# Performance work log

Measured on AMD Instinct MI355X. Metric: run time of the kernel, lower is better.

## Reference

```python
import jax, jax.numpy as jnp
import numpy as np

D = 4096  # in_features == out_features (required: LayerNorm(in_features) applied to out-dim output)
B, S = 4, 4096
LN_EPS = 1e-5


def setup_inputs() -> dict:
    key = jax.random.key(0)
    ks = jax.random.split(key, 5)
    return {
        "x": jax.random.normal(ks[0], (B, S, D), dtype=jnp.float32),
        "weight": jax.random.normal(ks[1], (D, D), dtype=jnp.float32),  # [out, in]
        "bias": jax.random.normal(ks[2], (D,), dtype=jnp.float32),
        "g": jax.random.normal(ks[3], (D,), dtype=jnp.float32),   # input scale [in]
        "h": jax.random.normal(ks[4], (D,), dtype=jnp.float32),   # output scale [out]
        "ln_gamma": jnp.ones((D,), dtype=jnp.float32),
        "ln_beta": jnp.zeros((D,), dtype=jnp.float32),
    }


def reference(x, weight, bias, g, h, ln_gamma, ln_beta):
    sign_w = jnp.sign(weight)                      # binarized weight [out, in]
    xg = x * g                                     # per-input-channel scale
    y = jnp.einsum("bsi,oi->bso", xg, sign_w) + bias
    y = y * h                                      # per-output-channel scale
    mu = jnp.mean(y, axis=-1, keepdims=True)
    var = jnp.mean(jnp.square(y - mu), axis=-1, keepdims=True)
    out = (y - mu) * jax.lax.rsqrt(var + LN_EPS) * ln_gamma + ln_beta
    return out
```

## Files before the change

### kernel.cpp

```cpp
#include <hip/hip_runtime.h>
#include <hip/hip_bf16.h>
#include <stdint.h>

typedef __bf16 bf16x8 __attribute__((ext_vector_type(8)));
typedef float f32x4 __attribute__((ext_vector_type(4)));

#define GLDS16(gp, lp) __builtin_amdgcn_global_load_lds( \
    (const __attribute__((address_space(1))) unsigned int*)(gp), \
    (__attribute__((address_space(3))) unsigned int*)(lp), 16, 0, 0)

#define BARRIER() asm volatile("s_barrier" ::: "memory")
#define VMCNT(n)  asm volatile("s_waitcnt vmcnt(" #n ")" ::: "memory")


__global__ __launch_bounds__(256) void prep_xg(
    const float* __restrict__ x, const float* __restrict__ g,
    __bf16* __restrict__ out, long total, int K)
{
    long i = ((long)blockIdx.x * blockDim.x + threadIdx.x) * 8;
    const long stride = (long)gridDim.x * blockDim.x * 8;
    for (; i < total; i += stride) {
        const int k = (int)(i & (long)(K - 1));
        f32x4 x0 = *(const f32x4*)(x + i);
        f32x4 x1 = *(const f32x4*)(x + i + 4);
        f32x4 g0 = *(const f32x4*)(g + k);
        f32x4 g1 = *(const f32x4*)(g + k + 4);
        bf16x8 o;
        #pragma unroll
        for (int j = 0; j < 4; ++j) o[j]     = (__bf16)(x0[j] * g0[j]);
        #pragma unroll
        for (int j = 0; j < 4; ++j) o[4 + j] = (__bf16)(x1[j] * g1[j]);
        *(bf16x8*)(out + i) = o;
    }
}

__global__ __launch_bounds__(256) void prep_sign(
    const float* __restrict__ w, __bf16* __restrict__ out, long total)
{
    long i = ((long)blockIdx.x * blockDim.x + threadIdx.x) * 8;
    const long stride = (long)gridDim.x * blockDim.x * 8;
    for (; i < total; i += stride) {
        f32x4 w0 = *(const f32x4*)(w + i);
        f32x4 w1 = *(const f32x4*)(w + i + 4);
        bf16x8 o;
        #pragma unroll
        for (int j = 0; j < 4; ++j)
            o[j]     = (__bf16)((w0[j] > 0.f) ? 1.f : ((w0[j] < 0.f) ? -1.f : 0.f));
        #pragma unroll
        for (int j = 0; j < 4; ++j)
            o[4 + j] = (__bf16)((w1[j] > 0.f) ? 1.f : ((w1[j] < 0.f) ? -1.f : 0.f));
        *(bf16x8*)(out + i) = o;
    }
}


template<bool BF16OUT>
__global__ __launch_bounds__(512, 2) void gemm_r4(
    const __bf16* __restrict__ A, const __bf16* __restrict__ B,
    const float* __restrict__ bias, const float* __restrict__ h,
    __bf16* __restrict__ yb, float* __restrict__ yf, int M, int N, int K)
{
    extern __shared__ __bf16 sm[];

    const int xcd = blockIdx.x & 7;
    const int l = blockIdx.x >> 3;
    const int bn = xcd * 2 + (l & 1);
    const int bm = l >> 1;

    const int t = threadIdx.x;
    const int lane = t & 63;
    const int w = t >> 6;
    const int wm = w >> 2;
    const int wn = w & 3;
    const int sl = lane >> 4;
    const int fr = lane & 15;
    const int swz = (sl ^ ((fr >> 1) & 3)) * 8;

    const int row8 = t >> 2;
    const int chS = ((t & 3) ^ ((t >> 3) & 3)) * 8;

    const __bf16* gA = A + (long)(bm * 256 + row8) * K + chS;
    const __bf16* gB = B + (long)(bn * 256 + row8) * K + chS;

    const int NT = K / 32;

#define STG_A(b, T) do { \
    GLDS16(gA + (long)(T) * 32,            &sm[(b) * 16384 + t * 8]); \
    GLDS16(gA + 128L * K + (long)(T) * 32, &sm[(b) * 16384 + 4096 + t * 8]); \
} while (0)
#define STG_B(b, T) do { \
    GLDS16(gB + (long)(T) * 32,            &sm[(b) * 16384 + 8192 + t * 8]); \
    GLDS16(gB + 128L * K + (long)(T) * 32, &sm[(b) * 16384 + 12288 + t * 8]); \
} while (0)

#define RD_A(dst, b, m)  dst = *(bf16x8*)&sm[(b) * 16384 + ((m) * 32 + wm * 16 + fr) * 32 + swz]
#define RD_B(dst, b, n)  dst = *(bf16x8*)&sm[(b) * 16384 + 8192 + ((n) * 64 + wn * 16 + fr) * 32 + swz]
#define MF(d, a, b) d = __builtin_amdgcn_mfma_f32_16x16x32_bf16(a, b, d, 0, 0, 0)

    f32x4 acc[8][4] = {};

    STG_A(0, 0); STG_B(0, 0);
    STG_A(1, 1); STG_B(1, 1);
    STG_A(2, 2); STG_B(2, 2);

    for (int ti = 0; ti < NT; ++ti) {
        const int b = ti & 3;

        if (ti < NT - 2)       VMCNT(8);
        else if (ti == NT - 2) VMCNT(4);
        else                   VMCNT(0);
        BARRIER();

        if (ti + 3 < NT) {
            const int bs = (ti + 3) & 3;
            STG_A(bs, ti + 3); STG_B(bs, ti + 3);
        }

        bf16x8 af[8], bf[4];
        #pragma unroll
        for (int m = 0; m < 8; ++m) RD_A(af[m], b, m);
        #pragma unroll
        for (int n = 0; n < 4; ++n) RD_B(bf[n], b, n);

        __builtin_amdgcn_s_setprio(1);
        #pragma unroll
        for (int m = 0; m < 8; ++m)
            #pragma unroll
            for (int n = 0; n < 4; ++n) MF(acc[m][n], af[m], bf[n]);
        __builtin_amdgcn_s_setprio(0);
    }

    const int cr = (lane >> 4) * 4;
    const int cc = lane & 15;
    #pragma unroll
    for (int n = 0; n < 4; ++n) {
        const int col = bn * 256 + n * 64 + wn * 16 + cc;
        const float bc = bias[col];
        const float hc = h[col];
        #pragma unroll
        for (int m = 0; m < 8; ++m) {
            const long rowb = (long)bm * 256 + m * 32 + wm * 16 + cr;
            #pragma unroll
            for (int j = 0; j < 4; ++j) {
                const float v = (acc[m][n][j] + bc) * hc;
                if (BF16OUT) {
                    union { __bf16 b; unsigned short u; } cv;
                    cv.b = (__bf16)v;
                    __builtin_nontemporal_store(cv.u,
                        (unsigned short*)yb + (rowb + j) * (long)N + col);
                } else {
                    __builtin_nontemporal_store(v, yf + (rowb + j) * (long)N + col);
                }
            }
        }
    }
#undef STG_A
#undef STG_B
#undef RD_A
#undef RD_B
#undef MF
}


__global__ __launch_bounds__(256) void ln_ws(
    const __bf16* __restrict__ ybuf, float* __restrict__ out,
    const float* __restrict__ gamma, const float* __restrict__ beta)
{
    const long r0 = (long)blockIdx.x * 2;
    const int t = threadIdx.x;
    const int lane = t & 63, wave = t >> 6;

    bf16x8 a0 = *(const bf16x8*)(ybuf + r0 * 4096 + t * 16);
    bf16x8 a1 = *(const bf16x8*)(ybuf + r0 * 4096 + t * 16 + 8);
    bf16x8 b0 = *(const bf16x8*)(ybuf + (r0 + 1) * 4096 + t * 16);
    bf16x8 b1 = *(const bf16x8*)(ybuf + (r0 + 1) * 4096 + t * 16 + 8);

    float v0[16], v1[16];
    float s0 = 0.f, q0 = 0.f, s1 = 0.f, q1 = 0.f;
    #pragma unroll
    for (int j = 0; j < 8; ++j) {
        v0[j] = (float)a0[j]; v0[8 + j] = (float)a1[j];
        v1[j] = (float)b0[j]; v1[8 + j] = (float)b1[j];
    }
    #pragma unroll
    for (int j = 0; j < 16; ++j) {
        s0 += v0[j]; q0 += v0[j] * v0[j];
        s1 += v1[j]; q1 += v1[j] * v1[j];
    }
    #pragma unroll
    for (int off = 32; off > 0; off >>= 1) {
        s0 += __shfl_down(s0, off); q0 += __shfl_down(q0, off);
        s1 += __shfl_down(s1, off); q1 += __shfl_down(q1, off);
    }
    __shared__ float red[4][4];
    if (lane == 0) { red[wave][0] = s0; red[wave][1] = q0; red[wave][2] = s1; red[wave][3] = q1; }
    __syncthreads();
    const float ts0 = red[0][0] + red[1][0] + red[2][0] + red[3][0];
    const float tq0 = red[0][1] + red[1][1] + red[2][1] + red[3][1];
    const float ts1 = red[0][2] + red[1][2] + red[2][2] + red[3][2];
    const float tq1 = red[0][3] + red[1][3] + red[2][3] + red[3][3];
    const float mu0 = ts0 * (1.0f / 4096.0f);
    const float mu1 = ts1 * (1.0f / 4096.0f);
    const float rs0 = rsqrtf(tq0 * (1.0f / 4096.0f) - mu0 * mu0 + 1e-5f);
    const float rs1 = rsqrtf(tq1 * (1.0f / 4096.0f) - mu1 * mu1 + 1e-5f);

    #pragma unroll
    for (int c = 0; c < 4; ++c) {
        f32x4 gv = *(const f32x4*)(gamma + t * 16 + c * 4);
        f32x4 bv = *(const f32x4*)(beta + t * 16 + c * 4);
        f32x4 o0, o1;
        #pragma unroll
        for (int j = 0; j < 4; ++j) {
            o0[j] = (v0[c * 4 + j] - mu0) * rs0 * gv[j] + bv[j];
            o1[j] = (v1[c * 4 + j] - mu1) * rs1 * gv[j] + bv[j];
        }
        *(f32x4*)(out + r0 * 4096 + t * 16 + c * 4) = o0;
        *(f32x4*)(out + (r0 + 1) * 4096 + t * 16 + c * 4) = o1;
    }
}


__global__ __launch_bounds__(256) void ln_inplace(
    float* __restrict__ y, const float* __restrict__ gamma,
    const float* __restrict__ beta, int N)
{
    const long row = blockIdx.x;
    float* p = y + row * (long)N;
    const int t = threadIdx.x;

    f32x4 v[4];
    float sum = 0.f, sq = 0.f;
    #pragma unroll
    for (int i = 0; i < 4; ++i) {
        v[i] = *(const f32x4*)(p + i * 1024 + t * 4);
        #pragma unroll
        for (int j = 0; j < 4; ++j) { sum += v[i][j]; sq += v[i][j] * v[i][j]; }
    }
    #pragma unroll
    for (int off = 32; off > 0; off >>= 1) {
        sum += __shfl_down(sum, off);
        sq  += __shfl_down(sq, off);
    }
    __shared__ float s1[4], s2[4];
    const int lane = t & 63, wave = t >> 6;
    if (lane == 0) { s1[wave] = sum; s2[wave] = sq; }
    __syncthreads();
    const float tot = s1[0] + s1[1] + s1[2] + s1[3];
    const float tsq = s2[0] + s2[1] + s2[2] + s2[3];
    const float mean = tot / (float)N;
    const float var = tsq / (float)N - mean * mean;
    const float rstd = rsqrtf(var + 1e-5f);

    #pragma unroll
    for (int i = 0; i < 4; ++i) {
        f32x4 ga = *(const f32x4*)(gamma + i * 1024 + t * 4);
        f32x4 be = *(const f32x4*)(beta + i * 1024 + t * 4);
        f32x4 o;
        #pragma unroll
        for (int j = 0; j < 4; ++j) o[j] = (v[i][j] - mean) * rstd * ga[j] + be[j];
        *(f32x4*)(p + i * 1024 + t * 4) = o;
    }
}


#define BMf 128
#define BNf 128
#define BKf 32
#define LDPf 40

__global__ __launch_bounds__(256) void binlin_gemm_fb(
    const float* __restrict__ x, const float* __restrict__ w,
    const float* __restrict__ bias, const float* __restrict__ g,
    const float* __restrict__ h, float* __restrict__ y,
    int M, int N, int K)
{
    __shared__ __bf16 As[BMf][LDPf];
    __shared__ __bf16 Bs[BNf][LDPf];
    const int nbn = N / BNf;
    const int bm = blockIdx.x / nbn;
    const int bn = blockIdx.x % nbn;
    const int t = threadIdx.x;
    const int lane = t & 63;
    const int wave = t >> 6;
    const int wm = wave >> 1, wn = wave & 1;
    const int row2 = t >> 2, kq = (t & 3) * 8;
    const long xbase = (long)bm * BMf * K;
    const long wbase = (long)bn * BNf * K;
    f32x4 acc[4][4] = {};
    const int fr = lane & 15;
    const int ko = (lane >> 4) * 8;
    for (int k0 = 0; k0 < K; k0 += BKf) {
        f32x4 ga = *(const f32x4*)(g + k0 + kq);
        f32x4 gb = *(const f32x4*)(g + k0 + kq + 4);
        #pragma unroll
        for (int p = 0; p < 2; ++p) {
            const int r = p * 64 + row2;
            const float* xp = x + xbase + (long)r * K + k0 + kq;
            f32x4 x0 = *(const f32x4*)xp;
            f32x4 x1 = *(const f32x4*)(xp + 4);
            bf16x8 av;
            #pragma unroll
            for (int i = 0; i < 4; ++i) av[i]     = (__bf16)(x0[i] * ga[i]);
            #pragma unroll
            for (int i = 0; i < 4; ++i) av[4 + i] = (__bf16)(x1[i] * gb[i]);
            *(bf16x8*)&As[r][kq] = av;
            const float* wp = w + wbase + (long)r * K + k0 + kq;
            f32x4 w0 = *(const f32x4*)wp;
            f32x4 w1 = *(const f32x4*)(wp + 4);
            bf16x8 bv;
            #pragma unroll
            for (int i = 0; i < 4; ++i)
                bv[i]     = (__bf16)((w0[i] > 0.f) ? 1.f : ((w0[i] < 0.f) ? -1.f : 0.f));
            #pragma unroll
            for (int i = 0; i < 4; ++i)
                bv[4 + i] = (__bf16)((w1[i] > 0.f) ? 1.f : ((w1[i] < 0.f) ? -1.f : 0.f));
            *(bf16x8*)&Bs[r][kq] = bv;
        }
        __syncthreads();
        bf16x8 af[4], bfr[4];
        #pragma unroll
        for (int m = 0; m < 4; ++m) af[m]  = *(bf16x8*)&As[wm * 64 + m * 16 + fr][ko];
        #pragma unroll
        for (int n = 0; n < 4; ++n) bfr[n] = *(bf16x8*)&Bs[wn * 64 + n * 16 + fr][ko];
        #pragma unroll
        for (int m = 0; m < 4; ++m)
            #pragma unroll
            for (int n = 0; n < 4; ++n)
                acc[m][n] = __builtin_amdgcn_mfma_f32_16x16x32_bf16(af[m], bfr[n], acc[m][n], 0, 0, 0);
        __syncthreads();
    }
    const int cr = (lane >> 4) * 4;
    const int cc = lane & 15;
    #pragma unroll
    for (int n = 0; n < 4; ++n) {
        const int col = bn * BNf + wn * 64 + n * 16 + cc;
        const float bc = bias[col];
        const float hc = h[col];
        #pragma unroll
        for (int m = 0; m < 4; ++m) {
            const long rowb = (long)bm * BMf + wm * 64 + m * 16 + cr;
            #pragma unroll
            for (int j = 0; j < 4; ++j)
                y[(rowb + j) * N + col] = (acc[m][n][j] + bc) * hc;
        }
    }
}

extern "C" void kernel_launch(void* const* d_in, const int* in_sizes, int n_in,
                              void* d_out, int out_size, void* d_ws, size_t ws_size,
                              hipStream_t stream)
{
    (void)n_in; (void)out_size;
    const float* x     = (const float*)d_in[0];
    const float* w     = (const float*)d_in[1];
    const float* bias  = (const float*)d_in[2];
    const float* g     = (const float*)d_in[3];
    const float* h     = (const float*)d_in[4];
    const float* gamma = (const float*)d_in[5];
    const float* beta  = (const float*)d_in[6];
    float* out = (float*)d_out;

    const int D = in_sizes[2];
    const long M = (long)in_sizes[0] / D;

    const size_t needA = (size_t)M * D * sizeof(__bf16);
    const size_t needB = (size_t)D * D * sizeof(__bf16);
    const size_t needY = (size_t)M * D * sizeof(__bf16);

    const bool okShape = (D == 4096 && (M % 512) == 0);

    if (okShape && ws_size >= needA + needB) {
        __bf16* xg   = (__bf16*)d_ws;
        __bf16* wsgn = (__bf16*)((char*)d_ws + needA);
        prep_xg  <<<dim3(2048), dim3(256), 0, stream>>>(x, g, xg, M * (long)D, D);
        prep_sign<<<dim3(2048), dim3(256), 0, stream>>>(w, wsgn, (long)D * D);
        dim3 grid((unsigned)((M / 256) * (D / 256)));

        if (ws_size >= needA + needB + needY) {
            __bf16* ybf = (__bf16*)((char*)d_ws + needA + needB);
            hipFuncSetAttribute((const void*)gemm_r4<true>,
                                hipFuncAttributeMaxDynamicSharedMemorySize, 131072);
            gemm_r4<true><<<grid, dim3(512), 131072, stream>>>(
                xg, wsgn, bias, h, ybf, nullptr, (int)M, D, D);
            ln_ws<<<dim3((unsigned)(M / 2)), dim3(256), 0, stream>>>(ybf, out, gamma, beta);
        } else {
            hipFuncSetAttribute((const void*)gemm_r4<false>,
                                hipFuncAttributeMaxDynamicSharedMemorySize, 131072);
            gemm_r4<false><<<grid, dim3(512), 131072, stream>>>(
                xg, wsgn, bias, h, nullptr, out, (int)M, D, D);
            ln_inplace<<<dim3((unsigned)M), dim3(256), 0, stream>>>(out, gamma, beta, D);
        }
    } else {
        dim3 grid((unsigned)((M / BMf) * (D / BNf)));
        binlin_gemm_fb<<<grid, dim3(256), 0, stream>>>(x, w, bias, g, h, out, (int)M, D, D);
        ln_inplace<<<dim3((unsigned)M), dim3(256), 0, stream>>>(out, gamma, beta, D);
    }
}
```

Measured before the change: 660.2 us.

## Shrink GEMM to 128x256 tiles with 4 waves and triple-buffered LDS

Replaces the 512-thread 256x256 tile GEMM with a 256-thread 128x256 tile kernel. Each wave now computes 64x128 (4x8 MFMA fragments), and the LDS ring drops from four stages to three with prefetch distance two. The grid doubles and per-block LDS shrinks from 128KB to 72KB, which may allow more resident blocks and better load balance. The cost is lower arithmetic intensity per tile, more redundant B loads across blocks, and shallower prefetch. The blockIdx-to-bn mapping is unchanged, so the bm range grows with the larger grid.

After: 724.7 us. +9.8%, slower.

```diff
diff --git a/kernel.cpp b/kernel.cpp
--- a/kernel.cpp
+++ b/kernel.cpp
@@ -55,7 +55,7 @@
 
 
 template<bool BF16OUT>
-__global__ __launch_bounds__(512, 2) void gemm_r4(
+__global__ __launch_bounds__(256, 2) void gemm_2b(
     const __bf16* __restrict__ A, const __bf16* __restrict__ B,
     const float* __restrict__ bias, const float* __restrict__ h,
     __bf16* __restrict__ yb, float* __restrict__ yf, int M, int N, int K)
@@ -70,8 +70,8 @@
     const int t = threadIdx.x;
     const int lane = t & 63;
     const int w = t >> 6;
-    const int wm = w >> 2;
-    const int wn = w & 3;
+    const int wm = w >> 1;
+    const int wn = w & 1;
     const int sl = lane >> 4;
     const int fr = lane & 15;
     const int swz = (sl ^ ((fr >> 1) & 3)) * 8;
@@ -79,67 +79,64 @@
     const int row8 = t >> 2;
     const int chS = ((t & 3) ^ ((t >> 3) & 3)) * 8;
 
-    const __bf16* gA = A + (long)(bm * 256 + row8) * K + chS;
+    const __bf16* gA = A + (long)(bm * 128 + row8) * K + chS;
     const __bf16* gB = B + (long)(bn * 256 + row8) * K + chS;
 
     const int NT = K / 32;
 
-#define STG_A(b, T) do { \
-    GLDS16(gA + (long)(T) * 32,            &sm[(b) * 16384 + t * 8]); \
-    GLDS16(gA + 128L * K + (long)(T) * 32, &sm[(b) * 16384 + 4096 + t * 8]); \
+#define STG(b, T) do { \
+    GLDS16(gA + (long)(T) * 32,           &sm[(b) * 12288 + t * 8]); \
+    GLDS16(gA + 64L * K + (long)(T) * 32, &sm[(b) * 12288 + 2048 + t * 8]); \
+    GLDS16(gB + (long)(T) * 32,           &sm[(b) * 12288 + 4096 + t * 8]); \
+    GLDS16(gB + 64L * K + (long)(T) * 32, &sm[(b) * 12288 + 6144 + t * 8]); \
+    GLDS16(gB + 128L * K + (long)(T) * 32, &sm[(b) * 12288 + 8192 + t * 8]); \
+    GLDS16(gB + 192L * K + (long)(T) * 32, &sm[(b) * 12288 + 10240 + t * 8]); \
 } while (0)
-#define STG_B(b, T) do { \
-    GLDS16(gB + (long)(T) * 32,            &sm[(b) * 16384 + 8192 + t * 8]); \
-    GLDS16(gB + 128L * K + (long)(T) * 32, &sm[(b) * 16384 + 12288 + t * 8]); \
-} while (0)
-
-#define RD_A(dst, b, m)  dst = *(bf16x8*)&sm[(b) * 16384 + ((m) * 32 + wm * 16 + fr) * 32 + swz]
-#define RD_B(dst, b, n)  dst = *(bf16x8*)&sm[(b) * 16384 + 8192 + ((n) * 64 + wn * 16 + fr) * 32 + swz]
+
+#define RD_A(dst, b, m)  dst = *(bf16x8*)&sm[(b) * 12288 + (wm * 64 + (m) * 16 + fr) * 32 + swz]
+#define RD_B(dst, b, n)  dst = *(bf16x8*)&sm[(b) * 12288 + 4096 + (wn * 128 + (n) * 16 + fr) * 32 + swz]
 #define MF(d, a, b) d = __builtin_amdgcn_mfma_f32_16x16x32_bf16(a, b, d, 0, 0, 0)
 
-    f32x4 acc[8][4] = {};
-
-    STG_A(0, 0); STG_B(0, 0);
-    STG_A(1, 1); STG_B(1, 1);
-    STG_A(2, 2); STG_B(2, 2);
-
+    f32x4 acc[4][8] = {};
+
+    STG(0, 0); STG(1, 1);
+
+    int b = 0;
     for (int ti = 0; ti < NT; ++ti) {
-        const int b = ti & 3;
-
-        if (ti < NT - 2)       VMCNT(8);
-        else if (ti == NT - 2) VMCNT(4);
-        else                   VMCNT(0);
+        if (ti < NT - 1) VMCNT(6); else VMCNT(0);
         BARRIER();
 
-        if (ti + 3 < NT) {
-            const int bs = (ti + 3) & 3;
-            STG_A(bs, ti + 3); STG_B(bs, ti + 3);
-        }
-
-        bf16x8 af[8], bf[4];
-        #pragma unroll
-        for (int m = 0; m < 8; ++m) RD_A(af[m], b, m);
-        #pragma unroll
-        for (int n = 0; n < 4; ++n) RD_B(bf[n], b, n);
+        if (ti + 2 < NT) {
+            const int bs = (b == 0) ? 2 : b - 1;
+            STG(bs, ti + 2);
+        }
+
+        bf16x8 af[4], bf[8];
+        #pragma unroll
+        for (int m = 0; m < 4; ++m) RD_A(af[m], b, m);
+        #pragma unroll
+        for (int n = 0; n < 8; ++n) RD_B(bf[n], b, n);
 
         __builtin_amdgcn_s_setprio(1);
         #pragma unroll
-        for (int m = 0; m < 8; ++m)
-            #pragma unroll
-            for (int n = 0; n < 4; ++n) MF(acc[m][n], af[m], bf[n]);
+        for (int m = 0; m < 4; ++m)
+            #pragma unroll
+            for (int n = 0; n < 8; ++n) MF(acc[m][n], af[m], bf[n]);
         __builtin_amdgcn_s_setprio(0);
+
+        b = (b == 2) ? 0 : b + 1;
     }
 
     const int cr = (lane >> 4) * 4;
     const int cc = lane & 15;
     #pragma unroll
-    for (int n = 0; n < 4; ++n) {
-        const int col = bn * 256 + n * 64 + wn * 16 + cc;
+    for (int n = 0; n < 8; ++n) {
+        const int col = bn * 256 + wn * 128 + n * 16 + cc;
         const float bc = bias[col];
         const float hc = h[col];
         #pragma unroll
-        for (int m = 0; m < 8; ++m) {
-            const long rowb = (long)bm * 256 + m * 32 + wm * 16 + cr;
+        for (int m = 0; m < 4; ++m) {
+            const long rowb = (long)bm * 128 + wm * 64 + m * 16 + cr;
             #pragma unroll
             for (int j = 0; j < 4; ++j) {
                 const float v = (acc[m][n][j] + bc) * hc;
@@ -154,8 +151,7 @@
             }
         }
     }
-#undef STG_A
-#undef STG_B
+#undef STG
 #undef RD_A
 #undef RD_B
 #undef MF
@@ -374,19 +370,19 @@
         __bf16* wsgn = (__bf16*)((char*)d_ws + needA);
         prep_xg  <<<dim3(2048), dim3(256), 0, stream>>>(x, g, xg, M * (long)D, D);
         prep_sign<<<dim3(2048), dim3(256), 0, stream>>>(w, wsgn, (long)D * D);
-        dim3 grid((unsigned)((M / 256) * (D / 256)));
+        dim3 grid((unsigned)((M / 128) * (D / 256)));
 
         if (ws_size >= needA + needB + needY) {
             __bf16* ybf = (__bf16*)((char*)d_ws + needA + needB);
-            hipFuncSetAttribute((const void*)gemm_r4<true>,
-                                hipFuncAttributeMaxDynamicSharedMemorySize, 131072);
-            gemm_r4<true><<<grid, dim3(512), 131072, stream>>>(
+            hipFuncSetAttribute((const void*)gemm_2b<true>,
+                                hipFuncAttributeMaxDynamicSharedMemorySize, 73728);
+            gemm_2b<true><<<grid, dim3(256), 73728, stream>>>(
                 xg, wsgn, bias, h, ybf, nullptr, (int)M, D, D);
             ln_ws<<<dim3((unsigned)(M / 2)), dim3(256), 0, stream>>>(ybf, out, gamma, beta);
         } else {
-            hipFuncSetAttribute((const void*)gemm_r4<false>,
-                                hipFuncAttributeMaxDynamicSharedMemorySize, 131072);
-            gemm_r4<false><<<grid, dim3(512), 131072, stream>>>(
+            hipFuncSetAttribute((const void*)gemm_2b<false>,
+                                hipFuncAttributeMaxDynamicSharedMemorySize, 73728);
+            gemm_2b<false><<<grid, dim3(256), 73728, stream>>>(
                 xg, wsgn, bias, h, nullptr, out, (int)M, D, D);
             ln_inplace<<<dim3((unsigned)M), dim3(256), 0, stream>>>(out, gamma, beta, D);
         }
```

## Split GEMM tile across 16 waves with 64x64 per-wave sub-tiles

Applied to the files above, without the earlier changes.

Doubles the GEMM workgroup from 512 to 1024 threads while keeping the 256x256 block tile. Each wave now owns a 64x64 output sub-tile instead of 128x64, which halves the accumulator registers and gives each thread a single LDS staging load per operand per K-step. The aim is more waves to hide memory and LDS latency. The launch bounds (1024, 4) impose a much tighter register budget that may force spills. The smaller per-wave tile also lowers the ratio of MFMA work to LDS reads.

Measured after the change: 676.8 us. 2.5% more time.

```diff
diff --git a/kernel.cpp b/kernel.cpp
--- a/kernel.cpp
+++ b/kernel.cpp
@@ -55,7 +55,7 @@
 
 
 template<bool BF16OUT>
-__global__ __launch_bounds__(512, 2) void gemm_r4(
+__global__ __launch_bounds__(1024, 4) void gemm_w4(
     const __bf16* __restrict__ A, const __bf16* __restrict__ B,
     const float* __restrict__ bias, const float* __restrict__ h,
     __bf16* __restrict__ yb, float* __restrict__ yf, int M, int N, int K)
@@ -84,47 +84,38 @@
 
     const int NT = K / 32;
 
-#define STG_A(b, T) do { \
-    GLDS16(gA + (long)(T) * 32,            &sm[(b) * 16384 + t * 8]); \
-    GLDS16(gA + 128L * K + (long)(T) * 32, &sm[(b) * 16384 + 4096 + t * 8]); \
+#define STG(b, T) do { \
+    GLDS16(gA + (long)(T) * 32, &sm[(b) * 16384 + t * 8]); \
+    GLDS16(gB + (long)(T) * 32, &sm[(b) * 16384 + 8192 + t * 8]); \
 } while (0)
-#define STG_B(b, T) do { \
-    GLDS16(gB + (long)(T) * 32,            &sm[(b) * 16384 + 8192 + t * 8]); \
-    GLDS16(gB + 128L * K + (long)(T) * 32, &sm[(b) * 16384 + 12288 + t * 8]); \
-} while (0)
-
-#define RD_A(dst, b, m)  dst = *(bf16x8*)&sm[(b) * 16384 + ((m) * 32 + wm * 16 + fr) * 32 + swz]
-#define RD_B(dst, b, n)  dst = *(bf16x8*)&sm[(b) * 16384 + 8192 + ((n) * 64 + wn * 16 + fr) * 32 + swz]
+
+#define RD_A(dst, b, m)  dst = *(bf16x8*)&sm[(b) * 16384 + (wm * 64 + (m) * 16 + fr) * 32 + swz]
+#define RD_B(dst, b, n)  dst = *(bf16x8*)&sm[(b) * 16384 + 8192 + (wn * 64 + (n) * 16 + fr) * 32 + swz]
 #define MF(d, a, b) d = __builtin_amdgcn_mfma_f32_16x16x32_bf16(a, b, d, 0, 0, 0)
 
-    f32x4 acc[8][4] = {};
-
-    STG_A(0, 0); STG_B(0, 0);
-    STG_A(1, 1); STG_B(1, 1);
-    STG_A(2, 2); STG_B(2, 2);
+    f32x4 acc[4][4] = {};
+
+    STG(0, 0); STG(1, 1); STG(2, 2);
 
     for (int ti = 0; ti < NT; ++ti) {
         const int b = ti & 3;
 
-        if (ti < NT - 2)       VMCNT(8);
-        else if (ti == NT - 2) VMCNT(4);
+        if (ti < NT - 2)       VMCNT(4);
+        else if (ti == NT - 2) VMCNT(2);
         else                   VMCNT(0);
         BARRIER();
 
-        if (ti + 3 < NT) {
-            const int bs = (ti + 3) & 3;
-            STG_A(bs, ti + 3); STG_B(bs, ti + 3);
-        }
-
-        bf16x8 af[8], bf[4];
-        #pragma unroll
-        for (int m = 0; m < 8; ++m) RD_A(af[m], b, m);
+        if (ti + 3 < NT) STG((ti + 3) & 3, ti + 3);
+
+        bf16x8 af[4], bf[4];
+        #pragma unroll
+        for (int m = 0; m < 4; ++m) RD_A(af[m], b, m);
         #pragma unroll
         for (int n = 0; n < 4; ++n) RD_B(bf[n], b, n);
 
         __builtin_amdgcn_s_setprio(1);
         #pragma unroll
-        for (int m = 0; m < 8; ++m)
+        for (int m = 0; m < 4; ++m)
             #pragma unroll
             for (int n = 0; n < 4; ++n) MF(acc[m][n], af[m], bf[n]);
         __builtin_amdgcn_s_setprio(0);
@@ -134,12 +125,12 @@
     const int cc = lane & 15;
     #pragma unroll
     for (int n = 0; n < 4; ++n) {
-        const int col = bn * 256 + n * 64 + wn * 16 + cc;
+        const int col = bn * 256 + wn * 64 + n * 16 + cc;
         const float bc = bias[col];
         const float hc = h[col];
         #pragma unroll
-        for (int m = 0; m < 8; ++m) {
-            const long rowb = (long)bm * 256 + m * 32 + wm * 16 + cr;
+        for (int m = 0; m < 4; ++m) {
+            const long rowb = (long)bm * 256 + wm * 64 + m * 16 + cr;
             #pragma unroll
             for (int j = 0; j < 4; ++j) {
                 const float v = (acc[m][n][j] + bc) * hc;
@@ -154,8 +145,7 @@
             }
         }
     }
-#undef STG_A
-#undef STG_B
+#undef STG
 #undef RD_A
 #undef RD_B
 #undef MF
@@ -378,15 +368,15 @@
 
         if (ws_size >= needA + needB + needY) {
             __bf16* ybf = (__bf16*)((char*)d_ws + needA + needB);
-            hipFuncSetAttribute((const void*)gemm_r4<true>,
+            hipFuncSetAttribute((const void*)gemm_w4<true>,
                                 hipFuncAttributeMaxDynamicSharedMemorySize, 131072);
-            gemm_r4<true><<<grid, dim3(512), 131072, stream>>>(
+            gemm_w4<true><<<grid, dim3(1024), 131072, stream>>>(
                 xg, wsgn, bias, h, ybf, nullptr, (int)M, D, D);
             ln_ws<<<dim3((unsigned)(M / 2)), dim3(256), 0, stream>>>(ybf, out, gamma, beta);
         } else {
-            hipFuncSetAttribute((const void*)gemm_r4<false>,
+            hipFuncSetAttribute((const void*)gemm_w4<false>,
                                 hipFuncAttributeMaxDynamicSharedMemorySize, 131072);
-            gemm_r4<false><<<grid, dim3(512), 131072, stream>>>(
+            gemm_w4<false><<<grid, dim3(1024), 131072, stream>>>(
                 xg, wsgn, bias, h, nullptr, out, (int)M, D, D);
             ln_inplace<<<dim3((unsigned)M), dim3(256), 0, stream>>>(out, gamma, beta, D);
         }
```
